# Performance work log

Hardware: AMD Instinct MI355X
Metric: run time of the kernel (lower is better)

## Reference

```python
import jax, jax.numpy as jnp
import numpy as np

B, S_T, P, D = 2, 8, 1369, 1024
S_STUDENT = 4
R = 128    # num_ref_samples
NS = 128   # num_shared_samples
K = 4      # topk
STUDENT_FRAMES = (0, 2, 4, 6)
EXTRA_FRAMES = (1, 3, 5, 7)   # teacher-only frames
HUBER_DELTA = 1.0
W1 = W2 = W3 = 1.0


def setup_inputs() -> dict:
    key = jax.random.key(0)
    k1, k2, k3, k4 = jax.random.split(key, 4)
    teacher_feats = jax.random.normal(k1, (B, S_T, P, D), dtype=jnp.float32)
    student_feats = jax.random.normal(k2, (B, S_STUDENT, P, D), dtype=jnp.float32)
    ref_perm = jax.random.permutation(k3, P)[:R].astype(jnp.int32)
    shared_perm = jax.random.permutation(k4, P)[:NS].astype(jnp.int32)
    return {"teacher_feats": teacher_feats, "student_feats": student_feats,
            "ref_perm": ref_perm, "shared_perm": shared_perm}


def _unit(x, eps):
    # F.normalize(x, dim=-1, eps=eps)
    n = jnp.linalg.norm(x, axis=-1, keepdims=True)
    return x / jnp.maximum(n, eps)


def _huber(pred, target):
    d = pred - target
    ad = jnp.abs(d)
    return jnp.where(ad < HUBER_DELTA, 0.5 * d * d, HUBER_DELTA * (ad - 0.5 * HUBER_DELTA))


def reference(teacher_feats, student_feats, ref_perm, shared_perm):
    t = jax.lax.stop_gradient(teacher_feats)  # teacher is always detached
    eps = 1e-8

    ref_t = t[:, STUDENT_FRAMES[0], ref_perm, :]        # [B,R,D]
    ref_s = student_feats[:, 0, ref_perm, :]            # [B,R,D]

    # top-K most similar teacher patches across extra frames
    extra_t = t[:, jnp.array(EXTRA_FRAMES)].reshape(B, len(EXTRA_FRAMES) * P, D)  # [B,M,D]
    sim = jnp.einsum('brd,bmd->brm', _unit(ref_t, 1e-12), _unit(extra_t, 1e-12))
    _, idx = jax.lax.top_k(sim, K)                      # [B,R,K]
    sim_high = jnp.take_along_axis(
        extra_t, idx.reshape(B, R * K)[:, :, None], axis=1).reshape(B, R, K, D)

    # vertex-ref / vertex-simhigh legs that don't depend on the shared frame
    b1_t = _unit(sim_high - ref_t[:, :, None, :], eps)  # [B,R,K,D]
    b1_s = _unit(sim_high - ref_s[:, :, None, :], eps)
    u2_t = _unit(ref_t[:, :, None, :] - sim_high, eps)  # [B,R,K,D]
    u2_s = _unit(ref_s[:, :, None, :] - sim_high, eps)

    s1 = jnp.float32(0.0)
    s2 = jnp.float32(0.0)
    s3 = jnp.float32(0.0)
    for f, t_idx in enumerate(STUDENT_FRAMES[1:]):
        sh_t = t[:, t_idx, shared_perm, :]              # [B,S,D]
        sh_s = student_feats[:, f + 1, shared_perm, :]  # [B,S,D]

        # angle1: vertex = ref; cos(shared-ref, simhigh-ref)
        a1_t = jnp.einsum('brsd,brkd->brsk', _unit(sh_t[:, None] - ref_t[:, :, None], eps), b1_t)
        a1_s = jnp.einsum('brsd,brkd->brsk', _unit(sh_s[:, None] - ref_s[:, :, None], eps), b1_s)
        s1 = s1 + _huber(a1_s, jax.lax.stop_gradient(a1_t)).sum()

        # angle2: vertex = sim_high; cos(ref-simhigh, shared-simhigh)
        v2_t = _unit(sh_t[:, None, :, None, :] - sim_high[:, :, None], eps)  # [B,R,S,K,D]
        v2_s = _unit(sh_s[:, None, :, None, :] - sim_high[:, :, None], eps)
        a2_t = jnp.einsum('brkd,brskd->brsk', u2_t, v2_t)
        a2_s = jnp.einsum('brkd,brskd->brsk', u2_s, v2_s)
        s2 = s2 + _huber(a2_s, jax.lax.stop_gradient(a2_t)).sum()

        # angle3: vertex = shared; cos(ref-shared, simhigh-shared)
        u3_t = _unit(ref_t[:, :, None] - sh_t[:, None], eps)                 # [B,R,S,D]
        u3_s = _unit(ref_s[:, :, None] - sh_s[:, None], eps)
        v3_t = _unit(sim_high[:, :, None] - sh_t[:, None, :, None, :], eps)  # [B,R,S,K,D]
        v3_s = _unit(sim_high[:, :, None] - sh_s[:, None, :, None, :], eps)
        a3_t = jnp.einsum('brsd,brskd->brsk', u3_t, v3_t)
        a3_s = jnp.einsum('brsd,brskd->brsk', u3_s, v3_s)
        s3 = s3 + _huber(a3_s, jax.lax.stop_gradient(a3_t)).sum()

    total = B * R * NS * K * len(STUDENT_FRAMES[1:])
    return W1 * s1 / total + W2 * s2 / total + W3 * s3 / total
```

## Files before the change

### kernel.cpp

```cpp
#include <hip/hip_runtime.h>
#include <float.h>

#define B_  2
#define ST_ 8
#define SS_ 4
#define P_  1369
#define D_  1024
#define R_  128
#define NS_ 128
#define K_  4
#define M_  5476

#define OFF_INVN  0u
#define OFF_REFT  11008u
#define OFF_REFS  (OFF_REFT + (unsigned)(B_*R_*D_))
#define OFF_PRRT  (OFF_REFS + (unsigned)(B_*R_*D_))
#define OFF_PRRS  (OFF_PRRT + 256u)
#define OFF_C     (OFF_PRRS + 256u)
#define OFF_IDX   (OFF_C + (unsigned)(B_*R_*M_))
#define OFF_PRST  (OFF_IDX + 1024u)
#define OFF_PRSS  (OFF_PRST + 1024u)
#define OFF_PSS   (OFF_PRSS + 1024u)
#define OFF_IB1T  (OFF_PSS + 1024u)
#define OFF_IB1S  (OFF_IB1T + 1024u)
#define OFF_NSH   (OFF_IB1S + 1024u)

__device__ __forceinline__ float dot4(const float4 a, const float4 b) {
  return a.x*b.x + a.y*b.y + a.z*b.z + a.w*b.w;
}

__global__ __launch_bounds__(256) void k_extra_norms(const float* __restrict__ teacher,
                                                     float* __restrict__ invn) {
  int row = blockIdx.x * 4 + (threadIdx.x >> 6);
  int lane = threadIdx.x & 63;
  if (row >= B_ * M_) return;
  int b = row / M_, m = row % M_;
  int j = m / P_, p = m % P_;
  const float* src = teacher + (((size_t)b * ST_ + 1 + 2 * j) * P_ + p) * D_;
  float s = 0.f;
  #pragma unroll
  for (int it = 0; it < 4; ++it) {
    float4 v = *(const float4*)(src + (it * 64 + lane) * 4);
    s += dot4(v, v);
  }
  for (int o = 32; o; o >>= 1) s += __shfl_down(s, o);
  if (lane == 0) invn[row] = 1.f / fmaxf(sqrtf(s), 1e-12f);
}

__global__ __launch_bounds__(256) void k_shnorm(const float* __restrict__ teacher,
                                                const float* __restrict__ student,
                                                const int* __restrict__ shared_perm,
                                                float* __restrict__ nsh) {
  int row = blockIdx.x * 4 + (threadIdx.x >> 6);
  int lane = threadIdx.x & 63;
  if (row >= 2 * B_ * 3 * NS_) return;
  int rid = row % (B_ * 3 * NS_);
  int is_stu = row / (B_ * 3 * NS_);
  int b = rid / (3 * NS_);
  int rem = rid % (3 * NS_);
  int f = rem / NS_, s = rem % NS_;
  int p = shared_perm[s];
  const float* src = is_stu
      ? student + (((size_t)b * SS_ + 1 + f) * P_ + p) * D_
      : teacher + (((size_t)b * ST_ + 2 + 2 * f) * P_ + p) * D_;
  float acc = 0.f;
  #pragma unroll
  for (int it = 0; it < 4; ++it) {
    float4 v = *(const float4*)(src + (it * 64 + lane) * 4);
    acc += dot4(v, v);
  }
  for (int o = 32; o; o >>= 1) acc += __shfl_down(acc, o);
  if (lane == 0) nsh[row] = acc;
}

__global__ __launch_bounds__(256) void k_ref_gather(const float* __restrict__ teacher,
                                                    const float* __restrict__ student,
                                                    const int* __restrict__ ref_perm,
                                                    float* __restrict__ reft,
                                                    float* __restrict__ refs,
                                                    float* __restrict__ prrt,
                                                    float* __restrict__ prrs) {
  int br = blockIdx.x;
  int b = br / R_, r = br % R_;
  int p = ref_perm[r];
  const float* st = teacher + (((size_t)b * ST_ + 0) * P_ + p) * D_;
  const float* ss = student + (((size_t)b * SS_ + 0) * P_ + p) * D_;
  float* dt = reft + (size_t)br * D_;
  float* dsp = refs + (size_t)br * D_;
  int t = threadIdx.x;
  float4 vt = *(const float4*)(st + t * 4);
  float4 vs = *(const float4*)(ss + t * 4);
  *(float4*)(dt + t * 4) = vt;
  *(float4*)(dsp + t * 4) = vs;
  float at = dot4(vt, vt);
  float as = dot4(vs, vs);
  for (int o = 32; o; o >>= 1) { at += __shfl_down(at, o); as += __shfl_down(as, o); }
  __shared__ float red[16];
  int w = t >> 6, lane = t & 63;
  if (lane == 0) { red[w] = at; red[8 + w] = as; }
  __syncthreads();
  if (t == 0) {
    prrt[br] = red[0] + red[1] + red[2] + red[3];
    prrs[br] = red[8] + red[9] + red[10] + red[11];
  }
}

__global__ __launch_bounds__(256) void k_sim_gemm(const float* __restrict__ teacher,
                                                  const float* __restrict__ reft,
                                                  float* __restrict__ C) {
  const int bid = blockIdx.x;
  const int kh  = bid & 1;
  const int rest = bid >> 1;
  const int b   = rest / 172;
  const int rem = rest % 172;
  const int rt  = rem / 86;
  const int mt  = rem % 86;
  const int r0 = rt * 64, m0 = mt * 64;
  __shared__ __align__(16) float Al[32 * 68];
  __shared__ __align__(16) float El[32 * 68];
  const int t = threadIdx.x;
  const int tx = t & 15, ty = t >> 4;
  const int lr = t >> 3;
  const int lk = (t & 7) * 4;
  const float* arow0 = reft + (size_t)(b * R_ + r0 + lr) * D_;
  const float* arow1 = reft + (size_t)(b * R_ + r0 + 32 + lr) * D_;
  const float* erow0; const float* erow1; bool ev0, ev1;
  {
    int m = m0 + lr; ev0 = m < M_;
    int mm = ev0 ? m : 0; int j = mm / P_, p = mm % P_;
    erow0 = teacher + (((size_t)b * ST_ + 1 + 2 * j) * P_ + p) * D_;
    m = m0 + 32 + lr; ev1 = m < M_;
    mm = ev1 ? m : 0; j = mm / P_; p = mm % P_;
    erow1 = teacher + (((size_t)b * ST_ + 1 + 2 * j) * P_ + p) * D_;
  }
  float acc[4][4];
  #pragma unroll
  for (int i = 0; i < 4; ++i)
    #pragma unroll
    for (int j = 0; j < 4; ++j) acc[i][j] = 0.f;

  const int kbeg = kh * 512, kend = kbeg + 512;
  for (int kc = kbeg; kc < kend; kc += 32) {
    __syncthreads();
    float4 a0 = *(const float4*)(arow0 + kc + lk);
    float4 a1 = *(const float4*)(arow1 + kc + lk);
    float4 e0 = ev0 ? *(const float4*)(erow0 + kc + lk) : make_float4(0, 0, 0, 0);
    float4 e1 = ev1 ? *(const float4*)(erow1 + kc + lk) : make_float4(0, 0, 0, 0);
    Al[(lk + 0) * 68 + lr] = a0.x; Al[(lk + 1) * 68 + lr] = a0.y;
    Al[(lk + 2) * 68 + lr] = a0.z; Al[(lk + 3) * 68 + lr] = a0.w;
    Al[(lk + 0) * 68 + 32 + lr] = a1.x; Al[(lk + 1) * 68 + 32 + lr] = a1.y;
    Al[(lk + 2) * 68 + 32 + lr] = a1.z; Al[(lk + 3) * 68 + 32 + lr] = a1.w;
    El[(lk + 0) * 68 + lr] = e0.x; El[(lk + 1) * 68 + lr] = e0.y;
    El[(lk + 2) * 68 + lr] = e0.z; El[(lk + 3) * 68 + lr] = e0.w;
    El[(lk + 0) * 68 + 32 + lr] = e1.x; El[(lk + 1) * 68 + 32 + lr] = e1.y;
    El[(lk + 2) * 68 + 32 + lr] = e1.z; El[(lk + 3) * 68 + 32 + lr] = e1.w;
    __syncthreads();
    #pragma unroll
    for (int kk = 0; kk < 32; ++kk) {
      float4 av = *(const float4*)&Al[kk * 68 + ty * 4];
      float4 ev = *(const float4*)&El[kk * 68 + tx * 4];
      acc[0][0] += av.x * ev.x; acc[0][1] += av.x * ev.y; acc[0][2] += av.x * ev.z; acc[0][3] += av.x * ev.w;
      acc[1][0] += av.y * ev.x; acc[1][1] += av.y * ev.y; acc[1][2] += av.y * ev.z; acc[1][3] += av.y * ev.w;
      acc[2][0] += av.z * ev.x; acc[2][1] += av.z * ev.y; acc[2][2] += av.z * ev.z; acc[2][3] += av.z * ev.w;
      acc[3][0] += av.w * ev.x; acc[3][1] += av.w * ev.y; acc[3][2] += av.w * ev.z; acc[3][3] += av.w * ev.w;
    }
  }
  const int mbase = m0 + tx * 4;
  #pragma unroll
  for (int i = 0; i < 4; ++i) {
    int r = r0 + ty * 4 + i;
    float* crow = C + (size_t)(b * R_ + r) * M_;
    #pragma unroll
    for (int q = 0; q < 4; ++q) {
      if (mbase + q < M_) atomicAdd(&crow[mbase + q], acc[i][q]);
    }
  }
}

__device__ __forceinline__ void topk_insert(float v, int m, float bv[4], int bi[4]) {
  bool better3 = (v > bv[3]) || (v == bv[3] && m < bi[3]);
  if (!better3) return;
  int pos = 3;
  while (pos > 0) {
    bool better = (v > bv[pos - 1]) || (v == bv[pos - 1] && m < bi[pos - 1]);
    if (better) { bv[pos] = bv[pos - 1]; bi[pos] = bi[pos - 1]; --pos; }
    else break;
  }
  bv[pos] = v; bi[pos] = m;
}

__global__ __launch_bounds__(256) void k_topk(const float* __restrict__ C,
                                              const float* __restrict__ invn,
                                              int* __restrict__ idxout) {
  int br = blockIdx.x;
  int b = br / R_;
  const float* row = C + (size_t)br * M_;
  const float* w = invn + (size_t)b * M_;
  int t = threadIdx.x;
  float bv[4] = {-FLT_MAX, -FLT_MAX, -FLT_MAX, -FLT_MAX};
  int   bi[4] = {0x7fffffff, 0x7fffffff, 0x7fffffff, 0x7fffffff};
  for (int m = t; m < M_; m += 256) topk_insert(row[m] * w[m], m, bv, bi);

  #pragma unroll
  for (int o = 1; o < 64; o <<= 1) {
    float ov[4]; int oi[4];
    #pragma unroll
    for (int q = 0; q < 4; ++q) {
      ov[q] = __shfl_xor(bv[q], o);
      oi[q] = __shfl_xor(bi[q], o);
    }
    #pragma unroll
    for (int q = 0; q < 4; ++q) topk_insert(ov[q], oi[q], bv, bi);
  }

  __shared__ float sv[16];
  __shared__ int   si[16];
  int wv = t >> 6, lane = t & 63;
  if (lane == 0) {
    #pragma unroll
    for (int q = 0; q < 4; ++q) { sv[wv * 4 + q] = bv[q]; si[wv * 4 + q] = bi[q]; }
  }
  __syncthreads();
  if (t == 0) {
    float tv[4] = {-FLT_MAX, -FLT_MAX, -FLT_MAX, -FLT_MAX};
    int   ti[4] = {0x7fffffff, 0x7fffffff, 0x7fffffff, 0x7fffffff};
    #pragma unroll
    for (int e = 0; e < 16; ++e) topk_insert(sv[e], si[e], tv, ti);
    #pragma unroll
    for (int q = 0; q < 4; ++q) idxout[br * 4 + q] = ti[q];
  }
}

__global__ __launch_bounds__(256) void k_prep(const float* __restrict__ teacher,
                                              const float* __restrict__ reft,
                                              const float* __restrict__ refs,
                                              const int* __restrict__ idx,
                                              float* __restrict__ prst,
                                              float* __restrict__ prss,
                                              float* __restrict__ pss,
                                              float* __restrict__ ib1t,
                                              float* __restrict__ ib1s) {
  int br = blockIdx.x;
  int b = br / R_;
  int w = threadIdx.x >> 6, lane = threadIdx.x & 63;
  int m = idx[br * 4 + w];
  int j = m / P_, p = m % P_;
  const float* sim = teacher + (((size_t)b * ST_ + 1 + 2 * j) * P_ + p) * D_;
  const float* rt = reft + (size_t)br * D_;
  const float* rs = refs + (size_t)br * D_;
  float s_ss = 0, s_rt = 0, s_rs = 0, s_dt = 0, s_ds = 0;
  #pragma unroll
  for (int it = 0; it < 4; ++it) {
    int d = (it * 64 + lane) * 4;
    float4 svv = *(const float4*)(sim + d);
    float4 tvv = *(const float4*)(rt + d);
    float4 uvv = *(const float4*)(rs + d);
    s_ss += dot4(svv, svv);
    s_rt += dot4(svv, tvv);
    s_rs += dot4(svv, uvv);
    float4 dt = make_float4(svv.x - tvv.x, svv.y - tvv.y, svv.z - tvv.z, svv.w - tvv.w);
    float4 ds = make_float4(svv.x - uvv.x, svv.y - uvv.y, svv.z - uvv.z, svv.w - uvv.w);
    s_dt += dot4(dt, dt);
    s_ds += dot4(ds, ds);
  }
  for (int o = 32; o; o >>= 1) {
    s_ss += __shfl_down(s_ss, o); s_rt += __shfl_down(s_rt, o); s_rs += __shfl_down(s_rs, o);
    s_dt += __shfl_down(s_dt, o); s_ds += __shfl_down(s_ds, o);
  }
  if (lane == 0) {
    int o = br * 4 + w;
    pss[o] = s_ss; prst[o] = s_rt; prss[o] = s_rs;
    ib1t[o] = 1.f / fmaxf(sqrtf(s_dt), 1e-8f);
    ib1s[o] = 1.f / fmaxf(sqrtf(s_ds), 1e-8f);
  }
}

__device__ __forceinline__ float huber1(float d) {
  float ad = fabsf(d);
  return (ad < 1.0f) ? 0.5f * d * d : (ad - 0.5f);
}

__global__ __launch_bounds__(256) void k_loss(const float* __restrict__ teacher,
                                              const float* __restrict__ student,
                                              const int* __restrict__ shared_perm,
                                              const int* __restrict__ idx,
                                              const float* __restrict__ reft,
                                              const float* __restrict__ refs,
                                              const float* __restrict__ prrt,
                                              const float* __restrict__ prrs,
                                              const float* __restrict__ prst,
                                              const float* __restrict__ prss,
                                              const float* __restrict__ pss,
                                              const float* __restrict__ ib1t,
                                              const float* __restrict__ ib1s,
                                              const float* __restrict__ nsh,
                                              float* __restrict__ out) {
  int br = blockIdx.x, f = blockIdx.y, sc = blockIdx.z;
  int b = br / R_;
  int tf = 2 + 2 * f;
  int sf = 1 + f;
  __shared__ __align__(16) float Lsim[4][1024];
  __shared__ __align__(16) float Lrt[1024];
  __shared__ __align__(16) float Lrs[1024];
  __shared__ int sperm[128];
  __shared__ float Lns[2][64];
  __shared__ float scal[22];
  __shared__ float wred[4];
  int t = threadIdx.x;
  {
    const float* rt = reft + (size_t)br * D_;
    const float* rs = refs + (size_t)br * D_;
    *(float4*)&Lrt[t * 4] = *(const float4*)(rt + t * 4);
    *(float4*)&Lrs[t * 4] = *(const float4*)(rs + t * 4);
    #pragma unroll
    for (int k = 0; k < 4; ++k) {
      int m = idx[br * 4 + k]; int j = m / P_, p = m % P_;
      const float* sim = teacher + (((size_t)b * ST_ + 1 + 2 * j) * P_ + p) * D_;
      *(float4*)&Lsim[k][t * 4] = *(const float4*)(sim + t * 4);
    }
  }
  if (t < 128) sperm[t] = shared_perm[t];
  if (t < 64) {
    int o = (b * 3 + f) * NS_ + sc * 64 + t;
    Lns[0][t] = nsh[o];
    Lns[1][t] = nsh[B_ * 3 * NS_ + o];
  }
  if (t < 4) {
    int o = br * 4 + t;
    scal[t] = prst[o]; scal[4 + t] = prss[o]; scal[8 + t] = pss[o];
    scal[12 + t] = ib1t[o]; scal[16 + t] = ib1s[o];
  }
  if (t == 4) scal[20] = prrt[br];
  if (t == 5) scal[21] = prrs[br];
  __syncthreads();

  const int g = t >> 2, gl = t & 3;
  const int s = sc * 64 + g;
  const int p = sperm[s];
  const float* sht = teacher + (((size_t)b * ST_ + tf) * P_ + p) * D_;
  const float* shs = student + (((size_t)b * SS_ + sf) * P_ + p) * D_;

  float qt0 = 0, qt1 = 0, qt2 = 0, qt3 = 0, qtr = 0;
  float qs0 = 0, qs1 = 0, qs2 = 0, qs3 = 0, qsr = 0;
  #pragma unroll 2
  for (int i = 0; i < 64; ++i) {
    int off = i * 16 + gl * 4;
    float4 a  = *(const float4*)(sht + off);
    float4 c  = *(const float4*)(shs + off);
    float4 v0 = *(const float4*)&Lsim[0][off];
    float4 v1 = *(const float4*)&Lsim[1][off];
    float4 v2 = *(const float4*)&Lsim[2][off];
    float4 v3 = *(const float4*)&Lsim[3][off];
    float4 r1 = *(const float4*)&Lrt[off];
    float4 r2 = *(const float4*)&Lrs[off];
    qt0 += dot4(a, v0); qt1 += dot4(a, v1); qt2 += dot4(a, v2); qt3 += dot4(a, v3);
    qtr += dot4(a, r1);
    qs0 += dot4(c, v0); qs1 += dot4(c, v1); qs2 += dot4(c, v2); qs3 += dot4(c, v3);
    qsr += dot4(c, r2);
  }
  #pragma unroll
  for (int o = 1; o <= 2; o <<= 1) {
    qt0 += __shfl_xor(qt0, o); qt1 += __shfl_xor(qt1, o);
    qt2 += __shfl_xor(qt2, o); qt3 += __shfl_xor(qt3, o);
    qtr += __shfl_xor(qtr, o);
    qs0 += __shfl_xor(qs0, o); qs1 += __shfl_xor(qs1, o);
    qs2 += __shfl_xor(qs2, o); qs3 += __shfl_xor(qs3, o);
    qsr += __shfl_xor(qsr, o);
  }
  const int k = gl;
  float qsim  = (gl == 0) ? qt0 : (gl == 1) ? qt1 : (gl == 2) ? qt2 : qt3;
  float qsimS = (gl == 0) ? qs0 : (gl == 1) ? qs1 : (gl == 2) ? qs2 : qs3;
  float qref = qtr, qrefS = qsr;
  float qss = Lns[0][g], qssS = Lns[1][g];

  float Prs_t = scal[k], Prs_s = scal[4 + k], Pss_k = scal[8 + k];
  float ibt = scal[12 + k], ibs = scal[16 + k];
  float Prr_t = scal[20], Prr_s = scal[21];
  float n1sq = qss - 2.f * qref + Prr_t;
  float i1 = 1.f / fmaxf(sqrtf(fmaxf(n1sq, 0.f)), 1e-8f);
  float n2sq = qss - 2.f * qsim + Pss_k;
  float i2 = 1.f / fmaxf(sqrtf(fmaxf(n2sq, 0.f)), 1e-8f);
  float a1t = (qsim - qref - Prs_t + Prr_t) * ibt * i1;
  float a2t = -(qsim - Pss_k - qref + Prs_t) * ibt * i2;
  float a3t = (qss - qsim - qref + Prs_t) * i1 * i2;
  float n1sqS = qssS - 2.f * qrefS + Prr_s;
  float i1s = 1.f / fmaxf(sqrtf(fmaxf(n1sqS, 0.f)), 1e-8f);
  float n2sqS = qssS - 2.f * qsimS + Pss_k;
  float i2s = 1.f / fmaxf(sqrtf(fmaxf(n2sqS, 0.f)), 1e-8f);
  float a1s = (qsimS - qrefS - Prs_s + Prr_s) * ibs * i1s;
  float a2s = -(qsimS - Pss_k - qrefS + Prs_s) * ibs * i2s;
  float a3s = (qssS - qsimS - qrefS + Prs_s) * i1s * i2s;
  float lacc = huber1(a1s - a1t) + huber1(a2s - a2t) + huber1(a3s - a3t);

  int w = t >> 6, lane = t & 63;
  for (int o = 32; o; o >>= 1) lacc += __shfl_down(lacc, o);
  if (lane == 0) wred[w] = lacc;
  __syncthreads();
  if (t == 0) {
    float ssum = wred[0] + wred[1] + wred[2] + wred[3];
    atomicAdd(out, ssum * (1.0f / 393216.0f));
  }
}

extern "C" void kernel_launch(void* const* d_in, const int* in_sizes, int n_in,
                              void* d_out, int out_size, void* d_ws, size_t ws_size,
                              hipStream_t stream) {
  const float* teacher = (const float*)d_in[0];
  const float* student = (const float*)d_in[1];
  const int* ref_perm = (const int*)d_in[2];
  const int* shared_perm = (const int*)d_in[3];
  float* ws = (float*)d_ws;
  float* invn = ws + OFF_INVN;
  float* reft = ws + OFF_REFT;
  float* refs = ws + OFF_REFS;
  float* prrt = ws + OFF_PRRT;
  float* prrs = ws + OFF_PRRS;
  float* C    = ws + OFF_C;
  int*   idx  = (int*)(ws + OFF_IDX);
  float* prst = ws + OFF_PRST;
  float* prss = ws + OFF_PRSS;
  float* pss  = ws + OFF_PSS;
  float* ib1t = ws + OFF_IB1T;
  float* ib1s = ws + OFF_IB1S;
  float* nsh  = ws + OFF_NSH;

  hipMemsetAsync(d_out, 0, sizeof(float), stream);
  hipMemsetAsync(C, 0, (size_t)B_ * R_ * M_ * sizeof(float), stream);

  k_extra_norms<<<(B_ * M_ + 3) / 4, 256, 0, stream>>>(teacher, invn);
  k_shnorm<<<(2 * B_ * 3 * NS_ + 3) / 4, 256, 0, stream>>>(teacher, student,
                                                           shared_perm, nsh);
  k_ref_gather<<<B_ * R_, 256, 0, stream>>>(teacher, student, ref_perm,
                                            reft, refs, prrt, prrs);
  k_sim_gemm<<<688, 256, 0, stream>>>(teacher, reft, C);
  k_topk<<<B_ * R_, 256, 0, stream>>>(C, invn, idx);
  k_prep<<<B_ * R_, 256, 0, stream>>>(teacher, reft, refs, idx,
                                      prst, prss, pss, ib1t, ib1s);
  k_loss<<<dim3(B_ * R_, 3, 2), 256, 0, stream>>>(teacher, student, shared_perm, idx,
                                                  reft, refs, prrt, prrs,
                                                  prst, prss, pss, ib1t, ib1s,
                                                  nsh, (float*)d_out);
}
```

Baseline: 343.1 us.

## Split sim GEMM K into four partial buffers, drop atomics and memset

```diff
diff --git a/kernel.cpp b/kernel.cpp
--- a/kernel.cpp
+++ b/kernel.cpp
@@ -13,17 +13,18 @@
 
 #define OFF_INVN  0u
 #define OFF_REFT  11008u
-#define OFF_REFS  (OFF_REFT + (unsigned)(B_*R_*D_))
-#define OFF_PRRT  (OFF_REFS + (unsigned)(B_*R_*D_))
+#define OFF_REFS  (OFF_REFT + 262144u)
+#define OFF_PRRT  (OFF_REFS + 262144u)
 #define OFF_PRRS  (OFF_PRRT + 256u)
-#define OFF_C     (OFF_PRRS + 256u)
-#define OFF_IDX   (OFF_C + (unsigned)(B_*R_*M_))
+#define OFF_IDX   (OFF_PRRS + 256u)
 #define OFF_PRST  (OFF_IDX + 1024u)
 #define OFF_PRSS  (OFF_PRST + 1024u)
 #define OFF_PSS   (OFF_PRSS + 1024u)
 #define OFF_IB1T  (OFF_PSS + 1024u)
 #define OFF_IB1S  (OFF_IB1T + 1024u)
 #define OFF_NSH   (OFF_IB1S + 1024u)
+#define OFF_C     (OFF_NSH + 1536u)
+#define CP_       1401856u
 
 __device__ __forceinline__ float dot4(const float4 a, const float4 b) {
   return a.x*b.x + a.y*b.y + a.z*b.z + a.w*b.w;
@@ -107,10 +108,10 @@
 
 __global__ __launch_bounds__(256) void k_sim_gemm(const float* __restrict__ teacher,
                                                   const float* __restrict__ reft,
-                                                  float* __restrict__ C) {
+                                                  float* __restrict__ Cp) {
   const int bid = blockIdx.x;
-  const int kh  = bid & 1;
-  const int rest = bid >> 1;
+  const int kq  = bid & 3;
+  const int rest = bid >> 2;
   const int b   = rest / 172;
   const int rem = rest % 172;
   const int rt  = rem / 86;
@@ -139,7 +140,7 @@
     #pragma unroll
     for (int j = 0; j < 4; ++j) acc[i][j] = 0.f;
 
-  const int kbeg = kh * 512, kend = kbeg + 512;
+  const int kbeg = kq * 256, kend = kbeg + 256;
   for (int kc = kbeg; kc < kend; kc += 32) {
     __syncthreads();
     float4 a0 = *(const float4*)(arow0 + kc + lk);
@@ -166,13 +167,18 @@
     }
   }
   const int mbase = m0 + tx * 4;
+  float* cbase = Cp + (size_t)kq * CP_;
   #pragma unroll
   for (int i = 0; i < 4; ++i) {
     int r = r0 + ty * 4 + i;
-    float* crow = C + (size_t)(b * R_ + r) * M_;
-    #pragma unroll
-    for (int q = 0; q < 4; ++q) {
-      if (mbase + q < M_) atomicAdd(&crow[mbase + q], acc[i][q]);
+    float* crow = cbase + (size_t)(b * R_ + r) * M_;
+    if (mbase + 3 < M_) {
+      *(float4*)(crow + mbase) = make_float4(acc[i][0], acc[i][1], acc[i][2], acc[i][3]);
+    } else {
+      if (mbase + 0 < M_) crow[mbase + 0] = acc[i][0];
+      if (mbase + 1 < M_) crow[mbase + 1] = acc[i][1];
+      if (mbase + 2 < M_) crow[mbase + 2] = acc[i][2];
+      if (mbase + 3 < M_) crow[mbase + 3] = acc[i][3];
     }
   }
 }
@@ -189,17 +195,23 @@
   bv[pos] = v; bi[pos] = m;
 }
 
-__global__ __launch_bounds__(256) void k_topk(const float* __restrict__ C,
+__global__ __launch_bounds__(256) void k_topk(const float* __restrict__ Cp,
                                               const float* __restrict__ invn,
                                               int* __restrict__ idxout) {
   int br = blockIdx.x;
   int b = br / R_;
-  const float* row = C + (size_t)br * M_;
+  const float* r0 = Cp + 0 * (size_t)CP_ + (size_t)br * M_;
+  const float* r1 = Cp + 1 * (size_t)CP_ + (size_t)br * M_;
+  const float* r2 = Cp + 2 * (size_t)CP_ + (size_t)br * M_;
+  const float* r3 = Cp + 3 * (size_t)CP_ + (size_t)br * M_;
   const float* w = invn + (size_t)b * M_;
   int t = threadIdx.x;
   float bv[4] = {-FLT_MAX, -FLT_MAX, -FLT_MAX, -FLT_MAX};
   int   bi[4] = {0x7fffffff, 0x7fffffff, 0x7fffffff, 0x7fffffff};
-  for (int m = t; m < M_; m += 256) topk_insert(row[m] * w[m], m, bv, bi);
+  for (int m = t; m < M_; m += 256) {
+    float v = ((r0[m] + r1[m]) + (r2[m] + r3[m])) * w[m];
+    topk_insert(v, m, bv, bi);
+  }
 
   #pragma unroll
   for (int o = 1; o < 64; o <<= 1) {
@@ -415,7 +427,6 @@
   float* refs = ws + OFF_REFS;
   float* prrt = ws + OFF_PRRT;
   float* prrs = ws + OFF_PRRS;
-  float* C    = ws + OFF_C;
   int*   idx  = (int*)(ws + OFF_IDX);
   float* prst = ws + OFF_PRST;
   float* prss = ws + OFF_PRSS;
@@ -423,17 +434,17 @@
   float* ib1t = ws + OFF_IB1T;
   float* ib1s = ws + OFF_IB1S;
   float* nsh  = ws + OFF_NSH;
+  float* Cp   = ws + OFF_C;
 
   hipMemsetAsync(d_out, 0, sizeof(float), stream);
-  hipMemsetAsync(C, 0, (size_t)B_ * R_ * M_ * sizeof(float), stream);
 
   k_extra_norms<<<(B_ * M_ + 3) / 4, 256, 0, stream>>>(teacher, invn);
   k_shnorm<<<(2 * B_ * 3 * NS_ + 3) / 4, 256, 0, stream>>>(teacher, student,
                                                            shared_perm, nsh);
   k_ref_gather<<<B_ * R_, 256, 0, stream>>>(teacher, student, ref_perm,
                                             reft, refs, prrt, prrs);
-  k_sim_gemm<<<688, 256, 0, stream>>>(teacher, reft, C);
-  k_topk<<<B_ * R_, 256, 0, stream>>>(C, invn, idx);
+  k_sim_gemm<<<1376, 256, 0, stream>>>(teacher, reft, Cp);
+  k_topk<<<B_ * R_, 256, 0, stream>>>(Cp, invn, idx);
   k_prep<<<B_ * R_, 256, 0, stream>>>(teacher, reft, refs, idx,
                                       prst, prss, pss, ib1t, ib1s);
   k_loss<<<dim3(B_ * R_, 3, 2), 256, 0, stream>>>(teacher, student, shared_perm, idx,
```

New measurement: 320.5 us. -6.6%, faster.
